# Performance work log

Measured on AMD Instinct MI355X. Metric: run time of the kernel, lower is better.

Reference implementation:

```python
import jax, jax.numpy as jnp
import numpy as np

N = 50000
E = 1600000
D_IN = 128
D_OUT = 128
K_EIG = 4
N_AGG = 3
N_SCALE = 3
AVG_D_LOG = float(np.log(33.0))  # avg_d['log'] for avg degree 32
BN_EPS = 1e-5


def setup_inputs() -> dict:
    key = jax.random.key(0)
    ks = jax.random.split(key, 8)
    h = jax.random.normal(ks[0], (N, D_IN), dtype=jnp.float32)
    eig = jax.random.normal(ks[1], (N, K_EIG), dtype=jnp.float32)
    snorm_n = jax.random.uniform(ks[2], (N, 1), dtype=jnp.float32)
    edge_src = jax.random.randint(ks[3], (E,), 0, N, dtype=jnp.int32)
    edge_dst = jax.random.randint(ks[4], (E,), 0, N, dtype=jnp.int32)
    d_cat = N_AGG * N_SCALE * D_IN  # 1152
    W = jax.random.normal(ks[5], (d_cat, D_OUT), dtype=jnp.float32) / np.sqrt(d_cat)
    b = jnp.zeros((D_OUT,), dtype=jnp.float32)
    bn_gamma = jnp.ones((D_OUT,), dtype=jnp.float32)
    bn_beta = jnp.zeros((D_OUT,), dtype=jnp.float32)
    bn_mean = jax.random.normal(ks[6], (D_OUT,), dtype=jnp.float32) * 0.1
    bn_var = jnp.ones((D_OUT,), dtype=jnp.float32)
    return {"h": h, "eig": eig, "snorm_n": snorm_n, "W": W, "b": b,
            "bn_gamma": bn_gamma, "bn_beta": bn_beta, "bn_mean": bn_mean,
            "bn_var": bn_var, "edge_src": edge_src, "edge_dst": edge_dst}


def reference(h, eig, snorm_n, W, b, bn_gamma, bn_beta, bn_mean, bn_var, edge_src, edge_dst):
    h_in = h
    # --- pretrans_edges: message e = src h; vector_field = eig_src - eig_dst ---
    h_e = h[edge_src]                      # [E, d] gathered edge messages
    vf = eig[edge_src] - eig[edge_dst]     # [E, k_eig]
    w = jnp.abs(vf[:, 0:1])                # dir1 weights [E, 1]

    # --- reduce: multi-aggregator segment reduce over destination nodes ---
    deg = jax.ops.segment_sum(jnp.ones((E,), h.dtype), edge_dst, num_segments=N)  # [N]
    deg_safe = jnp.maximum(deg, 1.0)
    sum_h = jax.ops.segment_sum(h_e, edge_dst, num_segments=N)
    mean_h = sum_h / deg_safe[:, None]
    max_h = jax.ops.segment_max(h_e, edge_dst, num_segments=N)
    max_h = jnp.where(deg[:, None] > 0, max_h, 0.0)  # empty mailbox -> 0
    dir_num = jax.ops.segment_sum(h_e * w, edge_dst, num_segments=N)
    dir_den = jax.ops.segment_sum(w, edge_dst, num_segments=N)  # [N, 1]
    dir_av = dir_num / (dir_den + 1e-30)
    agg = jnp.concatenate([mean_h, max_h, dir_av], axis=1)  # [N, 3d]

    # --- scalers: identity, amplification, attenuation ---
    logD = jnp.log(deg + 1.0)[:, None]
    amp = agg * (logD / AVG_D_LOG)
    att = agg * (AVG_D_LOG / jnp.maximum(logD, 1e-6))
    hcat = jnp.concatenate([agg, amp, att], axis=1)  # [N, 9d]

    # --- posttrans MLP (1 layer, no activation) ---
    out = hcat @ W + b
    # graph norm
    out = out * snorm_n
    # batch norm (eval mode, running stats)
    out = (out - bn_mean) * jax.lax.rsqrt(bn_var + BN_EPS) * bn_gamma + bn_beta
    out = jax.nn.relu(out)
    # residual (in_dim == out_dim)
    out = h_in + out
    # dropout p=0.0 / eval -> identity
    return out
```

## Files before the change

kernel.cpp:

```cpp
#include <hip/hip_runtime.h>
#include <hip/hip_bf16.h>

#define DIN 128
#define KEIG 4
#define BSH 7
#define BCAP 5120
#define ITEMS 16
#define AVG_D_LOG 3.4965075614664802f
#define BN_EPS 1e-5f

typedef __attribute__((ext_vector_type(8))) short bf16x8;
typedef __attribute__((ext_vector_type(4))) float f32x4;
typedef __attribute__((ext_vector_type(2))) float f32x2;

#define GLD16(SRC, DST) __builtin_amdgcn_global_load_lds(                     \
    (const __attribute__((address_space(1))) unsigned int*)(const void*)(SRC),\
    (__attribute__((address_space(3))) unsigned int*)(void*)(DST), 16, 0, 0)

static __device__ inline unsigned short f2bf(float f) {
    union { float f; unsigned u; } v; v.f = f;
    unsigned r = v.u + 0x7FFFu + ((v.u >> 16) & 1u);
    return (unsigned short)(r >> 16);
}
static __device__ inline unsigned pack2bf(float lo, float hi) {
    return (unsigned)f2bf(lo) | ((unsigned)f2bf(hi) << 16);
}
static __device__ inline f32x2 up2(unsigned u) {
    f32x2 r;
    r.x = __int_as_float(u << 16);
    r.y = __int_as_float(u & 0xffff0000u);
    return r;
}
static __device__ inline f32x2 pkmax(f32x2 a, f32x2 b) {
#if __has_builtin(__builtin_elementwise_max)
    return __builtin_elementwise_max(a, b);
#else
    a.x = fmaxf(a.x, b.x); a.y = fmaxf(a.y, b.y); return a;
#endif
}


__global__ void k_pb(const float* __restrict__ h, unsigned* __restrict__ hb,
                     const float* __restrict__ W, unsigned short* __restrict__ Wt,
                     const float* __restrict__ eig,
                     const int* __restrict__ src, const int* __restrict__ dst,
                     int* __restrict__ bcur, uint2* __restrict__ stag,
                     int nPairs, int wTotal, int E, int nbk, int gridB)
{
    __shared__ int lcnt[512];
    __shared__ int lbase[512];
    const int t = threadIdx.x;

    if ((int)blockIdx.x < gridB) {
        for (int b = t; b < nbk; b += 256) lcnt[b] = 0;
        __syncthreads();

        const int e0 = blockIdx.x * (256 * ITEMS);
        int   bky[ITEMS];
        int   rnk[ITEMS];
        uint2 rec[ITEMS];
#pragma unroll
        for (int k = 0; k < ITEMS; ++k) {
            const int e = e0 + t + k * 256;
            if (e < E) {
                const int s = src[e], d = dst[e];
                const float w = fabsf(eig[(size_t)s * KEIG] - eig[(size_t)d * KEIG]);
                rec[k] = make_uint2(((unsigned)f2bf(w) << 16) | (unsigned)s, (unsigned)d);
                bky[k] = d >> BSH;
                rnk[k] = atomicAdd(&lcnt[bky[k]], 1);
            } else bky[k] = -1;
        }
        __syncthreads();
        for (int b = t; b < nbk; b += 256) {
            const int c = lcnt[b];
            lbase[b] = c ? atomicAdd(&bcur[b], c) : 0;
        }
        __syncthreads();
#pragma unroll
        for (int k = 0; k < ITEMS; ++k) {
            if (bky[k] >= 0) {
                const int pos = lbase[bky[k]] + rnk[k];
                if (pos < BCAP) stag[(size_t)bky[k] * BCAP + pos] = rec[k];
            }
        }
    } else {
        const int i = ((int)blockIdx.x - gridB) * 256 + t;
        if (i < nPairs) {
            float2 v = reinterpret_cast<const float2*>(h)[i];
            hb[i] = pack2bf(v.x, v.y);
        }
        if (i < wTotal) {
            int k = i % 384;
            int rest = i / 384;
            int col = rest & 127;
            int s = rest >> 7;
            const int ks = k >> 5, kg = (k >> 3) & 3, ko = k & 7;
            const int c = s * 8 + kg * 2 + (col >> 6);
            const int lane = col & 63;
            const size_t idx = (size_t)ks * 12288 + c * 512 + lane * 8 + ko;
            Wt[idx] = f2bf(W[(s * 384 + k) * 128 + col]);
        }
    }
}


__global__ void k_group(const int* __restrict__ bcur, const uint2* __restrict__ stag,
                        unsigned* __restrict__ final_, int2* __restrict__ offcnt, int N)
{
    __shared__ uint2 sst[BCAP];
    __shared__ int hcnt[128];
    __shared__ int sbuf[2][128];
    const int b = blockIdx.x;
    const int t = threadIdx.x;
    const int cb = min(bcur[b], BCAP);

    for (int i = t; i < cb; i += 256) sst[i] = stag[(size_t)b * BCAP + i];
    if (t < 128) hcnt[t] = 0;
    __syncthreads();

    int dl[(BCAP + 255) / 256];
    int rk[(BCAP + 255) / 256];
    int nit = 0;
    for (int i = t; i < cb; i += 256) {
        const int d_loc = sst[i].y & 127;
        dl[nit] = d_loc;
        rk[nit] = atomicAdd(&hcnt[d_loc], 1);
        ++nit;
    }
    __syncthreads();

    int cur = 0;
    if (t < 128) sbuf[0][t] = hcnt[t];
    __syncthreads();
    for (int d = 1; d < 128; d <<= 1) {
        if (t < 128) {
            int x = sbuf[cur][t];
            if (t >= d) x += sbuf[cur][t - d];
            sbuf[cur ^ 1][t] = x;
        }
        cur ^= 1;
        __syncthreads();
    }
    const int exb = cur ^ 1;
    if (t < 128) sbuf[exb][t] = sbuf[cur][t] - hcnt[t];
    __syncthreads();

    if (t < 128) {
        const int dg = (b << BSH) + t;
        if (dg < N) offcnt[dg] = make_int2(b * BCAP + sbuf[exb][t], hcnt[t]);
    }
    nit = 0;
    for (int i = t; i < cb; i += 256) {
        final_[(size_t)b * BCAP + sbuf[exb][dl[nit]] + rk[nit]] = sst[i].x;
        ++nit;
    }
}


__global__ void k_prep(const float* __restrict__ h, unsigned* __restrict__ hb,
                       const float* __restrict__ W, unsigned short* __restrict__ Wt,
                       const float* __restrict__ eig, float* __restrict__ eig0,
                       int* __restrict__ cursor, int* __restrict__ bcur,
                       int nPairs, int wTotal, int N, int nbk)
{
    int i = blockIdx.x * 256 + threadIdx.x;
    if (i < nPairs) {
        float2 v = reinterpret_cast<const float2*>(h)[i];
        hb[i] = pack2bf(v.x, v.y);
    }
    if (i < wTotal) {
        int k = i % 384;
        int rest = i / 384;
        int col = rest & 127;
        int s = rest >> 7;
        const int ks = k >> 5, kg = (k >> 3) & 3, ko = k & 7;
        const int c = s * 8 + kg * 2 + (col >> 6);
        const int lane = col & 63;
        const size_t idx = (size_t)ks * 12288 + c * 512 + lane * 8 + ko;
        Wt[idx] = f2bf(W[(s * 384 + k) * 128 + col]);
    }
    if (i < N) {
        eig0[i] = eig[(size_t)i * KEIG];
        cursor[i] = 0;
    }
    if (i < nbk) bcur[i] = 0;
}

__global__ void k_hist(const int* __restrict__ dst, int* __restrict__ counts, int E) {
    int e = blockIdx.x * 256 + threadIdx.x;
    if (e < E) atomicAdd(&counts[dst[e]], 1);
}

__global__ void k_part(const int* __restrict__ counts, int* __restrict__ part, int N) {
    __shared__ int red[4];
    const int t = threadIdx.x;
    const int i = blockIdx.x * 256 + t;
    int v = (i < N) ? counts[i] : 0;
    for (int d = 32; d >= 1; d >>= 1) v += __shfl_down(v, d, 64);
    if ((t & 63) == 0) red[t >> 6] = v;
    __syncthreads();
    if (t == 0) part[blockIdx.x] = red[0] + red[1] + red[2] + red[3];
}

__global__ void k_scan1(const int* __restrict__ part, int* __restrict__ partoff,
                        int* __restrict__ total_out, int NB) {
    __shared__ int buf[2][256];
    const int t = threadIdx.x;
    int v = (t < NB) ? part[t] : 0;
    buf[0][t] = v;
    __syncthreads();
    int cur = 0;
    for (int d = 1; d < 256; d <<= 1) {
        int x = buf[cur][t];
        if (t >= d) x += buf[cur][t - d];
        buf[cur ^ 1][t] = x;
        cur ^= 1;
        __syncthreads();
    }
    if (t < NB) partoff[t] = buf[cur][t] - v;
    if (t == 255) *total_out = buf[cur][255];
}

__global__ void k_off(const int* __restrict__ counts, const int* __restrict__ partoff,
                      int* __restrict__ offsets, int* __restrict__ cursor, int N) {
    __shared__ int buf[2][256];
    const int t = threadIdx.x;
    const int i = blockIdx.x * 256 + t;
    int v = (i < N) ? counts[i] : 0;
    buf[0][t] = v;
    __syncthreads();
    int cur = 0;
    for (int d = 1; d < 256; d <<= 1) {
        int x = buf[cur][t];
        if (t >= d) x += buf[cur][t - d];
        buf[cur ^ 1][t] = x;
        cur ^= 1;
        __syncthreads();
    }
    if (i < N) {
        int excl = partoff[blockIdx.x] + buf[cur][t] - v;
        offsets[i] = excl;
        cursor[i]  = excl;
    }
}

__global__ void k_fill_csr(const int* __restrict__ src, const int* __restrict__ dst,
                           const float* __restrict__ eig0, int* __restrict__ cursor,
                           int2* __restrict__ sedge, int E)
{
    int e = blockIdx.x * 256 + threadIdx.x;
    if (e < E) {
        int s = src[e], d = dst[e];
        float w = fabsf(eig0[s] - eig0[d]);
        int pos = atomicAdd(&cursor[d], 1);
        sedge[pos] = make_int2(s, __float_as_int(w));
    }
}


template<bool PACKED>
__launch_bounds__(256, 4)
__global__ void k_agg(const unsigned* __restrict__ hb,
                      const int2* __restrict__ offcnt, const int* __restrict__ offsets,
                      const unsigned* __restrict__ upk, const int2* __restrict__ sedge,
                      unsigned short* __restrict__ agg, float2* __restrict__ scal, int N)
{
    const int tid = threadIdx.x;
    const int qid = tid >> 4;
    const int l16 = tid & 15;
    const int n = blockIdx.x * 16 + qid;
    if (n >= N) return;

    int e0, cnt;
    if (PACKED) { const int2 oc = offcnt[n]; e0 = oc.x; cnt = oc.y; }
    else        { e0 = offsets[n]; cnt = offsets[n + 1] - e0; }

    const uint4* __restrict__ hb4 = reinterpret_cast<const uint4*>(hb);

    f32x2 s2[4], m2[4], d2[4];
    float wsum = 0.f;
#pragma unroll
    for (int f = 0; f < 4; ++f) {
        s2[f] = (f32x2){0.f, 0.f};
        m2[f] = (f32x2){-INFINITY, -INFINITY};
        d2[f] = (f32x2){0.f, 0.f};
    }
    const int clampi = (cnt > 0) ? cnt - 1 : 0;

    uint4 bufA[8], bufB[8];
    float wvA[8], wvB[8];

#define STAGE(BUF, WV, BASE) do {                                        \
    _Pragma("unroll")                                                    \
    for (int j = 0; j < 8; ++j) {                                        \
        int ci = (BASE) + j; ci = ci < clampi ? ci : clampi;             \
        unsigned sidx;                                                   \
        if (PACKED) {                                                    \
            const unsigned u = upk[e0 + ci];                             \
            WV[j] = __int_as_float(u & 0xffff0000u);                     \
            sidx = (u & 0xffffu) << 4;                                   \
        } else {                                                         \
            const int2 v = sedge[e0 + ci];                               \
            WV[j] = __int_as_float(v.y);                                 \
            sidx = ((unsigned)v.x) << 4;                                 \
        }                                                                \
        BUF[j] = hb4[sidx | (unsigned)l16];                              \
    }                                                                    \
} while (0)

#define ACCUM(BUF, WV, BASE) do {                                        \
    _Pragma("unroll")                                                    \
    for (int j = 0; j < 8; ++j) {                                        \
        if ((BASE) + j < cnt) {                                          \
            const float wj = WV[j];                                      \
            const f32x2 wj2 = (f32x2){wj, wj};                           \
            const f32x2 p0 = up2(BUF[j].x), p1 = up2(BUF[j].y);          \
            const f32x2 p2 = up2(BUF[j].z), p3 = up2(BUF[j].w);          \
            s2[0] += p0; s2[1] += p1; s2[2] += p2; s2[3] += p3;          \
            m2[0] = pkmax(m2[0], p0); m2[1] = pkmax(m2[1], p1);          \
            m2[2] = pkmax(m2[2], p2); m2[3] = pkmax(m2[3], p3);          \
            d2[0] += p0 * wj2; d2[1] += p1 * wj2;                        \
            d2[2] += p2 * wj2; d2[3] += p3 * wj2;                        \
            wsum += wj;                                                  \
        }                                                                \
    }                                                                    \
} while (0)

    if (cnt > 0) {
        STAGE(bufA, wvA, 0);
        for (int base = 0; base < cnt; base += 16) {
            const bool haveB = (base + 8) < cnt;
            if (haveB) STAGE(bufB, wvB, base + 8);
            ACCUM(bufA, wvA, base);
            if (base + 16 < cnt) STAGE(bufA, wvA, base + 16);
            if (haveB) ACCUM(bufB, wvB, base + 8);
        }
    }
#undef STAGE
#undef ACCUM

    const float degf = (float)cnt;
    const float inv  = 1.0f / fmaxf(degf, 1.0f);
    const float dinv = 1.0f / (wsum + 1e-30f);
    const bool nz = (cnt > 0);
    uint4 pm, px, pd;
    pm.x = pack2bf(s2[0].x * inv, s2[0].y * inv);
    pm.y = pack2bf(s2[1].x * inv, s2[1].y * inv);
    pm.z = pack2bf(s2[2].x * inv, s2[2].y * inv);
    pm.w = pack2bf(s2[3].x * inv, s2[3].y * inv);
    px.x = pack2bf(nz ? m2[0].x : 0.f, nz ? m2[0].y : 0.f);
    px.y = pack2bf(nz ? m2[1].x : 0.f, nz ? m2[1].y : 0.f);
    px.z = pack2bf(nz ? m2[2].x : 0.f, nz ? m2[2].y : 0.f);
    px.w = pack2bf(nz ? m2[3].x : 0.f, nz ? m2[3].y : 0.f);
    pd.x = pack2bf(d2[0].x * dinv, d2[0].y * dinv);
    pd.y = pack2bf(d2[1].x * dinv, d2[1].y * dinv);
    pd.z = pack2bf(d2[2].x * dinv, d2[2].y * dinv);
    pd.w = pack2bf(d2[3].x * dinv, d2[3].y * dinv);

    uint4* aggv = reinterpret_cast<uint4*>(agg);
    const int mt = n >> 6, row = n & 63;
    const size_t b4 = (size_t)mt * 3072 + (size_t)(l16 & 3) * 64 + row;
    const int kshi = l16 >> 2;
    aggv[b4 + (size_t)(0 * 4 + kshi) * 256] = pm;
    aggv[b4 + (size_t)(1 * 4 + kshi) * 256] = px;
    aggv[b4 + (size_t)(2 * 4 + kshi) * 256] = pd;
    if (l16 == 0) {
        const float logD = logf(degf + 1.0f);
        scal[n] = make_float2(logD / AVG_D_LOG, AVG_D_LOG / fmaxf(logD, 1e-6f));
    }
}


__launch_bounds__(256, 2)
__global__ void k_mm(const unsigned short* __restrict__ agg, const float2* __restrict__ scal,
                     const float* __restrict__ h, const float* __restrict__ snorm,
                     const float* __restrict__ bvec, const float* __restrict__ gam,
                     const float* __restrict__ bet, const float* __restrict__ bmean,
                     const float* __restrict__ bvar, const unsigned short* __restrict__ Wt,
                     float* __restrict__ out, int N, int nT)
{
    __shared__ char smem[33792];
    unsigned short* As = (unsigned short*)smem;
    unsigned short* Bs = (unsigned short*)(smem + 8192);
    float* outS = (float*)smem;

    const int tid  = threadIdx.x;
    const int wave = tid >> 6;
    const int lane = tid & 63;
    const int r16  = lane & 15;
    const int kgrp = lane >> 4;
    const int cb = wave * 32;

    const int mt0 = blockIdx.x * 2;
    const int mt1 = (mt0 + 1 < nT) ? (mt0 + 1) : mt0;
    const char* aggb0 = (const char*)agg + (size_t)mt0 * 49152;
    const char* aggb1 = (const char*)agg + (size_t)mt1 * 49152;
    const char* wtbase = (const char*)Wt;

    auto stage = [&](int ks) {
        GLD16(aggb0 + (size_t)ks * 4096 + wave * 1024 + lane * 16,
              (char*)As + (size_t)wave * 1024);
        GLD16(aggb1 + (size_t)ks * 4096 + wave * 1024 + lane * 16,
              (char*)As + (size_t)(4 + wave) * 1024);
#pragma unroll
        for (int i = 0; i < 6; ++i) {
            const int c = wave * 6 + i;
            GLD16(wtbase + (size_t)ks * 24576 + (size_t)c * 1024 + lane * 16,
                  (char*)Bs + (size_t)c * 1024);
        }
    };

    f32x4 acc[2][4][2][3];
#pragma unroll
    for (int t = 0; t < 2; ++t)
#pragma unroll
        for (int m = 0; m < 4; ++m)
#pragma unroll
            for (int ct = 0; ct < 2; ++ct)
#pragma unroll
                for (int sv = 0; sv < 3; ++sv)
                    acc[t][m][ct][sv] = (f32x4){0.f, 0.f, 0.f, 0.f};

    for (int ks = 0; ks < 12; ++ks) {
        if (ks) __syncthreads();
        stage(ks);
        __syncthreads();

        bf16x8 a0[4], a1[4], b[6];
#pragma unroll
        for (int m = 0; m < 4; ++m) {
            a0[m] = *reinterpret_cast<const bf16x8*>(
                &As[((size_t)kgrp * 64 + m * 16 + r16) * 8]);
            a1[m] = *reinterpret_cast<const bf16x8*>(
                &As[((size_t)(4 + kgrp) * 64 + m * 16 + r16) * 8]);
        }
#pragma unroll
        for (int sv = 0; sv < 3; ++sv)
#pragma unroll
            for (int ct = 0; ct < 2; ++ct)
                b[sv * 2 + ct] = *reinterpret_cast<const bf16x8*>(
                    &Bs[(((size_t)sv * 4 + kgrp) * 128 + cb + ct * 16 + r16) * 8]);
#pragma unroll
        for (int sv = 0; sv < 3; ++sv)
#pragma unroll
            for (int ct = 0; ct < 2; ++ct)
#pragma unroll
                for (int m = 0; m < 4; ++m) {
                    acc[0][m][ct][sv] = __builtin_amdgcn_mfma_f32_16x16x32_bf16(
                        a0[m], b[sv * 2 + ct], acc[0][m][ct][sv], 0, 0, 0);
                    acc[1][m][ct][sv] = __builtin_amdgcn_mfma_f32_16x16x32_bf16(
                        a1[m], b[sv * 2 + ct], acc[1][m][ct][sv], 0, 0, 0);
                }
    }

    __syncthreads();
#pragma unroll
    for (int t = 0; t < 2; ++t) {
        if (t == 1 && mt1 == mt0) break;
        const int nb = (t ? mt1 : mt0) * 64;
#pragma unroll
        for (int ct = 0; ct < 2; ++ct) {
            const int col = cb + ct * 16 + r16;
            const float bc  = bvec[col];
            const float mc  = bmean[col];
            const float rs  = rsqrtf(bvar[col] + BN_EPS);
            const float gc  = gam[col];
            const float bec = bet[col];
#pragma unroll
            for (int m = 0; m < 4; ++m) {
#pragma unroll
                for (int r = 0; r < 4; ++r) {
                    const int row = m * 16 + kgrp * 4 + r;
                    const int n  = nb + row;
                    float sn = 0.f; float2 sc = make_float2(0.f, 0.f);
                    if (n < N) { sn = snorm[n]; sc = scal[n]; }
                    float v = acc[t][m][ct][0][r] + sc.x * acc[t][m][ct][1][r]
                                                  + sc.y * acc[t][m][ct][2][r];
                    float y = (v + bc) * sn;
                    y = (y - mc) * rs * gc + bec;
                    y = fmaxf(y, 0.f);
                    outS[row * 132 + col] = y;
                }
            }
        }
        __syncthreads();
        const int rows = (N - nb < 64) ? (N - nb) : 64;
#pragma unroll
        for (int it = 0; it < 8; ++it) {
            const int idx = it * 256 + tid;
            const int row = idx >> 5;
            const int c4  = idx & 31;
            if (row < rows) {
                const float4 hv = *reinterpret_cast<const float4*>(
                    &h[(size_t)(nb + row) * 128 + c4 * 4]);
                float4 yv = *reinterpret_cast<const float4*>(&outS[row * 132 + c4 * 4]);
                yv.x += hv.x; yv.y += hv.y; yv.z += hv.z; yv.w += hv.w;
                *reinterpret_cast<float4*>(&out[(size_t)(nb + row) * 128 + c4 * 4]) = yv;
            }
        }
        __syncthreads();
    }
}


extern "C" void kernel_launch(void* const* d_in, const int* in_sizes, int n_in,
                              void* d_out, int out_size, void* d_ws, size_t ws_size,
                              hipStream_t stream)
{
    const float* h     = (const float*)d_in[0];
    const float* eig   = (const float*)d_in[1];
    const float* snorm = (const float*)d_in[2];
    const float* W     = (const float*)d_in[3];
    const float* bvec  = (const float*)d_in[4];
    const float* gam   = (const float*)d_in[5];
    const float* bet   = (const float*)d_in[6];
    const float* bmean = (const float*)d_in[7];
    const float* bvar  = (const float*)d_in[8];
    const int*   esrc  = (const int*)d_in[9];
    const int*   edst  = (const int*)d_in[10];
    float* out = (float*)d_out;

    const int N = in_sizes[0] / DIN;
    const int E = in_sizes[9];
    const int NB = (N + 255) / 256;
    const int nPairs = N * DIN / 2;
    const int wTotal = 3 * 128 * 384;
    const int nbk = (N + 127) >> BSH;
    const int N64 = (N + 63) / 64;
    const int N128 = (N + 127) / 128;
    (void)ws_size; (void)n_in; (void)out_size;

    char* base = (char*)d_ws;
    size_t o = 0;
    auto take = [&](size_t bytes) {
        char* p = base + o;
        o = (o + bytes + 255) & ~(size_t)255;
        return p;
    };
    unsigned* hb       = (unsigned*)take((size_t)nPairs * 4);
    unsigned short* Wt = (unsigned short*)take((size_t)wTotal * 2);
    float* eig0        = (float*)take((size_t)N * 4);
    int* cursor        = (int*)take((size_t)(N + 1) * 4);
    float2* scal       = (float2*)take((size_t)N * 8);

    const size_t agg_bytes  = (size_t)N64 * 49152;
    const size_t stag_bytes = (size_t)nbk * BCAP * 8;
    const size_t shared_bytes = agg_bytes > stag_bytes ? agg_bytes : stag_bytes;

    const size_t bucket_bytes = (size_t)nbk * BCAP * 4
                              + (size_t)N * 8
                              + (size_t)nbk * 4
                              + shared_bytes + 8192;
    const bool bucketOK = (N <= 65536) && (nbk <= 512) && ((o + bucket_bytes) <= ws_size);

    const int gridPrep = (nPairs + 255) / 256;
    const int gridE    = (E + 255) / 256;
    const int gridB    = (E + 256 * ITEMS - 1) / (256 * ITEMS);
    const int gridN16  = (N + 15) / 16;

    if (bucketOK) {
        unsigned* fin   = (unsigned*)take((size_t)nbk * BCAP * 4);
        int2* offcnt    = (int2*)take((size_t)N * 8);
        int* bcur       = (int*)take((size_t)nbk * 4);
        char* shared    = take(shared_bytes);
        uint2* stag     = (uint2*)shared;
        unsigned short* agg = (unsigned short*)shared;

        hipMemsetAsync(bcur, 0, (size_t)nbk * 4, stream);
        k_pb<<<gridB + gridPrep, 256, 0, stream>>>(h, hb, W, Wt, eig, esrc, edst,
                                                   bcur, stag, nPairs, wTotal, E,
                                                   nbk, gridB);
        k_group<<<nbk, 256, 0, stream>>>(bcur, stag, fin, offcnt, N);
        k_agg<true><<<gridN16, 256, 0, stream>>>(hb, offcnt, nullptr, fin, nullptr,
                                                 agg, scal, N);
        k_mm<<<N128, 256, 0, stream>>>(agg, scal, h, snorm, bvec, gam, bet, bmean, bvar,
                                       Wt, out, N, N64);
    } else {
        int* counts  = (int*)take((size_t)(N + 1) * 4);
        int* offsets = (int*)take((size_t)(N + 1) * 4);
        int2* sedge  = (int2*)take((size_t)(E + 16) * 8);
        int* part    = (int*)take((size_t)NB * 4);
        int* partoff = (int*)take((size_t)NB * 4);
        int* bcur    = (int*)take(4096);
        unsigned short* agg = (unsigned short*)take(agg_bytes);

        k_prep<<<gridPrep, 256, 0, stream>>>(h, hb, W, Wt, eig, eig0, counts, bcur,
                                             nPairs, wTotal, N, 1);
        k_hist<<<gridE, 256, 0, stream>>>(edst, counts, E);
        k_part<<<NB, 256, 0, stream>>>(counts, part, N);
        k_scan1<<<1, 256, 0, stream>>>(part, partoff, &offsets[N], NB);
        k_off<<<NB, 256, 0, stream>>>(counts, partoff, offsets, cursor, N);
        k_fill_csr<<<gridE, 256, 0, stream>>>(esrc, edst, eig0, cursor, sedge, E);
        k_agg<false><<<gridN16, 256, 0, stream>>>(hb, nullptr, offsets, nullptr, sedge,
                                                  agg, scal, N);
        k_mm<<<N128, 256, 0, stream>>>(agg, scal, h, snorm, bvec, gam, bet, bmean, bvar,
                                       Wt, out, N, N64);
    }
}
```

Baseline: 151.8 us.

## Fuse bucket grouping with neighbor aggregation and shrink staging records

After: 167.3 us. 1.1x slower.

```diff
diff --git a/kernel.cpp b/kernel.cpp
--- a/kernel.cpp
+++ b/kernel.cpp
@@ -44,7 +44,8 @@
                      const float* __restrict__ W, unsigned short* __restrict__ Wt,
                      const float* __restrict__ eig,
                      const int* __restrict__ src, const int* __restrict__ dst,
-                     int* __restrict__ bcur, uint2* __restrict__ stag,
+                     int* __restrict__ bcur, unsigned* __restrict__ stagW,
+                     unsigned char* __restrict__ stagD,
                      int nPairs, int wTotal, int E, int nbk, int gridB)
 {
     __shared__ int lcnt[512];
@@ -56,16 +57,18 @@
         __syncthreads();
 
         const int e0 = blockIdx.x * (256 * ITEMS);
-        int   bky[ITEMS];
-        int   rnk[ITEMS];
-        uint2 rec[ITEMS];
+        int      bky[ITEMS];
+        int      rnk[ITEMS];
+        unsigned rw[ITEMS];
+        int      rd[ITEMS];
 #pragma unroll
         for (int k = 0; k < ITEMS; ++k) {
             const int e = e0 + t + k * 256;
             if (e < E) {
                 const int s = src[e], d = dst[e];
                 const float w = fabsf(eig[(size_t)s * KEIG] - eig[(size_t)d * KEIG]);
-                rec[k] = make_uint2(((unsigned)f2bf(w) << 16) | (unsigned)s, (unsigned)d);
+                rw[k] = ((unsigned)f2bf(w) << 16) | (unsigned)s;
+                rd[k] = d & ((1 << BSH) - 1);
                 bky[k] = d >> BSH;
                 rnk[k] = atomicAdd(&lcnt[bky[k]], 1);
             } else bky[k] = -1;
@@ -80,7 +83,10 @@
         for (int k = 0; k < ITEMS; ++k) {
             if (bky[k] >= 0) {
                 const int pos = lbase[bky[k]] + rnk[k];
-                if (pos < BCAP) stag[(size_t)bky[k] * BCAP + pos] = rec[k];
+                if (pos < BCAP) {
+                    stagW[(size_t)bky[k] * BCAP + pos] = rw[k];
+                    stagD[(size_t)bky[k] * BCAP + pos] = (unsigned char)rd[k];
+                }
             }
         }
     } else {
@@ -104,17 +110,26 @@
 }
 
 
-__global__ void k_group(const int* __restrict__ bcur, const uint2* __restrict__ stag,
-                        unsigned* __restrict__ final_, int2* __restrict__ offcnt, int N)
+__launch_bounds__(256)
+__global__ void k_ga(const unsigned* __restrict__ hb, const int* __restrict__ bcur,
+                     const unsigned* __restrict__ stagW,
+                     const unsigned char* __restrict__ stagD,
+                     unsigned short* __restrict__ agg, float2* __restrict__ scal, int N)
 {
-    __shared__ uint2 sst[BCAP];
+    __shared__ unsigned sW[BCAP];
+    __shared__ unsigned grpW[BCAP];
+    __shared__ unsigned char sD[BCAP];
     __shared__ int hcnt[128];
     __shared__ int sbuf[2][128];
+
     const int b = blockIdx.x;
     const int t = threadIdx.x;
     const int cb = min(bcur[b], BCAP);
 
-    for (int i = t; i < cb; i += 256) sst[i] = stag[(size_t)b * BCAP + i];
+    for (int i = t; i < cb; i += 256) {
+        sW[i] = stagW[(size_t)b * BCAP + i];
+        sD[i] = stagD[(size_t)b * BCAP + i];
+    }
     if (t < 128) hcnt[t] = 0;
     __syncthreads();
 
@@ -122,7 +137,7 @@
     int rk[(BCAP + 255) / 256];
     int nit = 0;
     for (int i = t; i < cb; i += 256) {
-        const int d_loc = sst[i].y & 127;
+        const int d_loc = sD[i];
         dl[nit] = d_loc;
         rk[nit] = atomicAdd(&hcnt[d_loc], 1);
         ++nit;
@@ -145,166 +160,45 @@
     if (t < 128) sbuf[exb][t] = sbuf[cur][t] - hcnt[t];
     __syncthreads();
 
-    if (t < 128) {
-        const int dg = (b << BSH) + t;
-        if (dg < N) offcnt[dg] = make_int2(b * BCAP + sbuf[exb][t], hcnt[t]);
-    }
     nit = 0;
     for (int i = t; i < cb; i += 256) {
-        final_[(size_t)b * BCAP + sbuf[exb][dl[nit]] + rk[nit]] = sst[i].x;
+        grpW[sbuf[exb][dl[nit]] + rk[nit]] = sW[i];
         ++nit;
     }
-}
-
-
-__global__ void k_prep(const float* __restrict__ h, unsigned* __restrict__ hb,
-                       const float* __restrict__ W, unsigned short* __restrict__ Wt,
-                       const float* __restrict__ eig, float* __restrict__ eig0,
-                       int* __restrict__ cursor, int* __restrict__ bcur,
-                       int nPairs, int wTotal, int N, int nbk)
-{
-    int i = blockIdx.x * 256 + threadIdx.x;
-    if (i < nPairs) {
-        float2 v = reinterpret_cast<const float2*>(h)[i];
-        hb[i] = pack2bf(v.x, v.y);
-    }
-    if (i < wTotal) {
-        int k = i % 384;
-        int rest = i / 384;
-        int col = rest & 127;
-        int s = rest >> 7;
-        const int ks = k >> 5, kg = (k >> 3) & 3, ko = k & 7;
-        const int c = s * 8 + kg * 2 + (col >> 6);
-        const int lane = col & 63;
-        const size_t idx = (size_t)ks * 12288 + c * 512 + lane * 8 + ko;
-        Wt[idx] = f2bf(W[(s * 384 + k) * 128 + col]);
-    }
-    if (i < N) {
-        eig0[i] = eig[(size_t)i * KEIG];
-        cursor[i] = 0;
-    }
-    if (i < nbk) bcur[i] = 0;
-}
-
-__global__ void k_hist(const int* __restrict__ dst, int* __restrict__ counts, int E) {
-    int e = blockIdx.x * 256 + threadIdx.x;
-    if (e < E) atomicAdd(&counts[dst[e]], 1);
-}
-
-__global__ void k_part(const int* __restrict__ counts, int* __restrict__ part, int N) {
-    __shared__ int red[4];
-    const int t = threadIdx.x;
-    const int i = blockIdx.x * 256 + t;
-    int v = (i < N) ? counts[i] : 0;
-    for (int d = 32; d >= 1; d >>= 1) v += __shfl_down(v, d, 64);
-    if ((t & 63) == 0) red[t >> 6] = v;
-    __syncthreads();
-    if (t == 0) part[blockIdx.x] = red[0] + red[1] + red[2] + red[3];
-}
-
-__global__ void k_scan1(const int* __restrict__ part, int* __restrict__ partoff,
-                        int* __restrict__ total_out, int NB) {
-    __shared__ int buf[2][256];
-    const int t = threadIdx.x;
-    int v = (t < NB) ? part[t] : 0;
-    buf[0][t] = v;
-    __syncthreads();
-    int cur = 0;
-    for (int d = 1; d < 256; d <<= 1) {
-        int x = buf[cur][t];
-        if (t >= d) x += buf[cur][t - d];
-        buf[cur ^ 1][t] = x;
-        cur ^= 1;
-        __syncthreads();
-    }
-    if (t < NB) partoff[t] = buf[cur][t] - v;
-    if (t == 255) *total_out = buf[cur][255];
-}
-
-__global__ void k_off(const int* __restrict__ counts, const int* __restrict__ partoff,
-                      int* __restrict__ offsets, int* __restrict__ cursor, int N) {
-    __shared__ int buf[2][256];
-    const int t = threadIdx.x;
-    const int i = blockIdx.x * 256 + t;
-    int v = (i < N) ? counts[i] : 0;
-    buf[0][t] = v;
-    __syncthreads();
-    int cur = 0;
-    for (int d = 1; d < 256; d <<= 1) {
-        int x = buf[cur][t];
-        if (t >= d) x += buf[cur][t - d];
-        buf[cur ^ 1][t] = x;
-        cur ^= 1;
-        __syncthreads();
-    }
-    if (i < N) {
-        int excl = partoff[blockIdx.x] + buf[cur][t] - v;
-        offsets[i] = excl;
-        cursor[i]  = excl;
-    }
-}
-
-__global__ void k_fill_csr(const int* __restrict__ src, const int* __restrict__ dst,
-                           const float* __restrict__ eig0, int* __restrict__ cursor,
-                           int2* __restrict__ sedge, int E)
-{
-    int e = blockIdx.x * 256 + threadIdx.x;
-    if (e < E) {
-        int s = src[e], d = dst[e];
-        float w = fabsf(eig0[s] - eig0[d]);
-        int pos = atomicAdd(&cursor[d], 1);
-        sedge[pos] = make_int2(s, __float_as_int(w));
-    }
-}
-
-
-template<bool PACKED>
-__launch_bounds__(256, 4)
-__global__ void k_agg(const unsigned* __restrict__ hb,
-                      const int2* __restrict__ offcnt, const int* __restrict__ offsets,
-                      const unsigned* __restrict__ upk, const int2* __restrict__ sedge,
-                      unsigned short* __restrict__ agg, float2* __restrict__ scal, int N)
-{
-    const int tid = threadIdx.x;
-    const int qid = tid >> 4;
-    const int l16 = tid & 15;
-    const int n = blockIdx.x * 16 + qid;
-    if (n >= N) return;
-
-    int e0, cnt;
-    if (PACKED) { const int2 oc = offcnt[n]; e0 = oc.x; cnt = oc.y; }
-    else        { e0 = offsets[n]; cnt = offsets[n + 1] - e0; }
-
+    __syncthreads();
+
+    const int qid = t >> 4;
+    const int l16 = t & 15;
     const uint4* __restrict__ hb4 = reinterpret_cast<const uint4*>(hb);
-
-    f32x2 s2[4], m2[4], d2[4];
-    float wsum = 0.f;
-#pragma unroll
-    for (int f = 0; f < 4; ++f) {
-        s2[f] = (f32x2){0.f, 0.f};
-        m2[f] = (f32x2){-INFINITY, -INFINITY};
-        d2[f] = (f32x2){0.f, 0.f};
-    }
-    const int clampi = (cnt > 0) ? cnt - 1 : 0;
-
-    uint4 bufA[8], bufB[8];
-    float wvA[8], wvB[8];
+    uint4* aggv = reinterpret_cast<uint4*>(agg);
+
+    for (int round = 0; round < 8; ++round) {
+        const int row = round * 16 + qid;
+        const int n = (b << BSH) + row;
+        if (n >= N) continue;
+        const int e0  = sbuf[exb][row];
+        const int cnt = hcnt[row];
+
+        f32x2 s2[4], m2[4], d2[4];
+        float wsum = 0.f;
+#pragma unroll
+        for (int f = 0; f < 4; ++f) {
+            s2[f] = (f32x2){0.f, 0.f};
+            m2[f] = (f32x2){-INFINITY, -INFINITY};
+            d2[f] = (f32x2){0.f, 0.f};
+        }
+        const int clampi = (cnt > 0) ? cnt - 1 : 0;
+
+        uint4 bufA[8], bufB[8];
+        float wvA[8], wvB[8];
 
 #define STAGE(BUF, WV, BASE) do {                                        \
     _Pragma("unroll")                                                    \
     for (int j = 0; j < 8; ++j) {                                        \
         int ci = (BASE) + j; ci = ci < clampi ? ci : clampi;             \
-        unsigned sidx;                                                   \
-        if (PACKED) {                                                    \
-            const unsigned u = upk[e0 + ci];                             \
-            WV[j] = __int_as_float(u & 0xffff0000u);                     \
-            sidx = (u & 0xffffu) << 4;                                   \
-        } else {                                                         \
-            const int2 v = sedge[e0 + ci];                               \
-            WV[j] = __int_as_float(v.y);                                 \
-            sidx = ((unsigned)v.x) << 4;                                 \
-        }                                                                \
-        BUF[j] = hb4[sidx | (unsigned)l16];                              \
+        const unsigned u = grpW[e0 + ci];                                \
+        WV[j] = __int_as_float(u & 0xffff0000u);                         \
+        BUF[j] = hb4[((u & 0xffffu) << 4) | (unsigned)l16];              \
     }                                                                    \
 } while (0)
 
@@ -326,6 +220,210 @@
     }                                                                    \
 } while (0)
 
+        if (cnt > 0) {
+            STAGE(bufA, wvA, 0);
+            for (int base = 0; base < cnt; base += 16) {
+                const bool haveB = (base + 8) < cnt;
+                if (haveB) STAGE(bufB, wvB, base + 8);
+                ACCUM(bufA, wvA, base);
+                if (base + 16 < cnt) STAGE(bufA, wvA, base + 16);
+                if (haveB) ACCUM(bufB, wvB, base + 8);
+            }
+        }
+#undef STAGE
+#undef ACCUM
+
+        const float degf = (float)cnt;
+        const float inv  = 1.0f / fmaxf(degf, 1.0f);
+        const float dinv = 1.0f / (wsum + 1e-30f);
+        const bool nz = (cnt > 0);
+        uint4 pm, px, pd;
+        pm.x = pack2bf(s2[0].x * inv, s2[0].y * inv);
+        pm.y = pack2bf(s2[1].x * inv, s2[1].y * inv);
+        pm.z = pack2bf(s2[2].x * inv, s2[2].y * inv);
+        pm.w = pack2bf(s2[3].x * inv, s2[3].y * inv);
+        px.x = pack2bf(nz ? m2[0].x : 0.f, nz ? m2[0].y : 0.f);
+        px.y = pack2bf(nz ? m2[1].x : 0.f, nz ? m2[1].y : 0.f);
+        px.z = pack2bf(nz ? m2[2].x : 0.f, nz ? m2[2].y : 0.f);
+        px.w = pack2bf(nz ? m2[3].x : 0.f, nz ? m2[3].y : 0.f);
+        pd.x = pack2bf(d2[0].x * dinv, d2[0].y * dinv);
+        pd.y = pack2bf(d2[1].x * dinv, d2[1].y * dinv);
+        pd.z = pack2bf(d2[2].x * dinv, d2[2].y * dinv);
+        pd.w = pack2bf(d2[3].x * dinv, d2[3].y * dinv);
+
+        const int mt = n >> 6, rowm = n & 63;
+        const size_t b4 = (size_t)mt * 3072 + (size_t)(l16 & 3) * 64 + rowm;
+        const int kshi = l16 >> 2;
+        aggv[b4 + (size_t)(0 * 4 + kshi) * 256] = pm;
+        aggv[b4 + (size_t)(1 * 4 + kshi) * 256] = px;
+        aggv[b4 + (size_t)(2 * 4 + kshi) * 256] = pd;
+        if (l16 == 0) {
+            const float logD = logf(degf + 1.0f);
+            scal[n] = make_float2(logD / AVG_D_LOG, AVG_D_LOG / fmaxf(logD, 1e-6f));
+        }
+    }
+}
+
+
+__global__ void k_prep(const float* __restrict__ h, unsigned* __restrict__ hb,
+                       const float* __restrict__ W, unsigned short* __restrict__ Wt,
+                       const float* __restrict__ eig, float* __restrict__ eig0,
+                       int* __restrict__ cursor, int* __restrict__ bcur,
+                       int nPairs, int wTotal, int N, int nbk)
+{
+    int i = blockIdx.x * 256 + threadIdx.x;
+    if (i < nPairs) {
+        float2 v = reinterpret_cast<const float2*>(h)[i];
+        hb[i] = pack2bf(v.x, v.y);
+    }
+    if (i < wTotal) {
+        int k = i % 384;
+        int rest = i / 384;
+        int col = rest & 127;
+        int s = rest >> 7;
+        const int ks = k >> 5, kg = (k >> 3) & 3, ko = k & 7;
+        const int c = s * 8 + kg * 2 + (col >> 6);
+        const int lane = col & 63;
+        const size_t idx = (size_t)ks * 12288 + c * 512 + lane * 8 + ko;
+        Wt[idx] = f2bf(W[(s * 384 + k) * 128 + col]);
+    }
+    if (i < N) {
+        eig0[i] = eig[(size_t)i * KEIG];
+        cursor[i] = 0;
+    }
+    if (i < nbk) bcur[i] = 0;
+}
+
+__global__ void k_hist(const int* __restrict__ dst, int* __restrict__ counts, int E) {
+    int e = blockIdx.x * 256 + threadIdx.x;
+    if (e < E) atomicAdd(&counts[dst[e]], 1);
+}
+
+__global__ void k_part(const int* __restrict__ counts, int* __restrict__ part, int N) {
+    __shared__ int red[4];
+    const int t = threadIdx.x;
+    const int i = blockIdx.x * 256 + t;
+    int v = (i < N) ? counts[i] : 0;
+    for (int d = 32; d >= 1; d >>= 1) v += __shfl_down(v, d, 64);
+    if ((t & 63) == 0) red[t >> 6] = v;
+    __syncthreads();
+    if (t == 0) part[blockIdx.x] = red[0] + red[1] + red[2] + red[3];
+}
+
+__global__ void k_scan1(const int* __restrict__ part, int* __restrict__ partoff,
+                        int* __restrict__ total_out, int NB) {
+    __shared__ int buf[2][256];
+    const int t = threadIdx.x;
+    int v = (t < NB) ? part[t] : 0;
+    buf[0][t] = v;
+    __syncthreads();
+    int cur = 0;
+    for (int d = 1; d < 256; d <<= 1) {
+        int x = buf[cur][t];
+        if (t >= d) x += buf[cur][t - d];
+        buf[cur ^ 1][t] = x;
+        cur ^= 1;
+        __syncthreads();
+    }
+    if (t < NB) partoff[t] = buf[cur][t] - v;
+    if (t == 255) *total_out = buf[cur][255];
+}
+
+__global__ void k_off(const int* __restrict__ counts, const int* __restrict__ partoff,
+                      int* __restrict__ offsets, int* __restrict__ cursor, int N) {
+    __shared__ int buf[2][256];
+    const int t = threadIdx.x;
+    const int i = blockIdx.x * 256 + t;
+    int v = (i < N) ? counts[i] : 0;
+    buf[0][t] = v;
+    __syncthreads();
+    int cur = 0;
+    for (int d = 1; d < 256; d <<= 1) {
+        int x = buf[cur][t];
+        if (t >= d) x += buf[cur][t - d];
+        buf[cur ^ 1][t] = x;
+        cur ^= 1;
+        __syncthreads();
+    }
+    if (i < N) {
+        int excl = partoff[blockIdx.x] + buf[cur][t] - v;
+        offsets[i] = excl;
+        cursor[i]  = excl;
+    }
+}
+
+__global__ void k_fill_csr(const int* __restrict__ src, const int* __restrict__ dst,
+                           const float* __restrict__ eig0, int* __restrict__ cursor,
+                           int2* __restrict__ sedge, int E)
+{
+    int e = blockIdx.x * 256 + threadIdx.x;
+    if (e < E) {
+        int s = src[e], d = dst[e];
+        float w = fabsf(eig0[s] - eig0[d]);
+        int pos = atomicAdd(&cursor[d], 1);
+        sedge[pos] = make_int2(s, __float_as_int(w));
+    }
+}
+
+__launch_bounds__(256, 4)
+__global__ void k_agg_csr(const unsigned* __restrict__ hb,
+                          const int* __restrict__ offsets, const int2* __restrict__ sedge,
+                          unsigned short* __restrict__ agg, float2* __restrict__ scal, int N)
+{
+    const int tid = threadIdx.x;
+    const int qid = tid >> 4;
+    const int l16 = tid & 15;
+    const int n = blockIdx.x * 16 + qid;
+    if (n >= N) return;
+
+    const int e0 = offsets[n];
+    const int cnt = offsets[n + 1] - e0;
+
+    const uint4* __restrict__ hb4 = reinterpret_cast<const uint4*>(hb);
+
+    f32x2 s2[4], m2[4], d2[4];
+    float wsum = 0.f;
+#pragma unroll
+    for (int f = 0; f < 4; ++f) {
+        s2[f] = (f32x2){0.f, 0.f};
+        m2[f] = (f32x2){-INFINITY, -INFINITY};
+        d2[f] = (f32x2){0.f, 0.f};
+    }
+    const int clampi = (cnt > 0) ? cnt - 1 : 0;
+    const int safe = (cnt > 0);
+
+    uint4 bufA[8], bufB[8];
+    float wvA[8], wvB[8];
+
+#define STAGE(BUF, WV, BASE) do {                                        \
+    _Pragma("unroll")                                                    \
+    for (int j = 0; j < 8; ++j) {                                        \
+        int ci = (BASE) + j; ci = ci < clampi ? ci : clampi;             \
+        const int2 v = sedge[e0 + ci];                                   \
+        WV[j] = __int_as_float(v.y);                                     \
+        const unsigned sidx = ((unsigned)(safe ? v.x : 0)) << 4;         \
+        BUF[j] = hb4[sidx | (unsigned)l16];                              \
+    }                                                                    \
+} while (0)
+
+#define ACCUM(BUF, WV, BASE) do {                                        \
+    _Pragma("unroll")                                                    \
+    for (int j = 0; j < 8; ++j) {                                        \
+        if ((BASE) + j < cnt) {                                          \
+            const float wj = WV[j];                                      \
+            const f32x2 wj2 = (f32x2){wj, wj};                           \
+            const f32x2 p0 = up2(BUF[j].x), p1 = up2(BUF[j].y);          \
+            const f32x2 p2 = up2(BUF[j].z), p3 = up2(BUF[j].w);          \
+            s2[0] += p0; s2[1] += p1; s2[2] += p2; s2[3] += p3;          \
+            m2[0] = pkmax(m2[0], p0); m2[1] = pkmax(m2[1], p1);          \
+            m2[2] = pkmax(m2[2], p2); m2[3] = pkmax(m2[3], p3);          \
+            d2[0] += p0 * wj2; d2[1] += p1 * wj2;                        \
+            d2[2] += p2 * wj2; d2[3] += p3 * wj2;                        \
+            wsum += wj;                                                  \
+        }                                                                \
+    }                                                                    \
+} while (0)
+
     if (cnt > 0) {
         STAGE(bufA, wvA, 0);
         for (int base = 0; base < cnt; base += 16) {
@@ -543,14 +641,12 @@
     int* cursor        = (int*)take((size_t)(N + 1) * 4);
     float2* scal       = (float2*)take((size_t)N * 8);
 
-    const size_t agg_bytes  = (size_t)N64 * 49152;
-    const size_t stag_bytes = (size_t)nbk * BCAP * 8;
-    const size_t shared_bytes = agg_bytes > stag_bytes ? agg_bytes : stag_bytes;
+    const size_t agg_bytes = (size_t)N64 * 49152;
 
     const size_t bucket_bytes = (size_t)nbk * BCAP * 4
-                              + (size_t)N * 8
+                              + (size_t)nbk * BCAP
                               + (size_t)nbk * 4
-                              + shared_bytes + 8192;
+                              + agg_bytes + 8192;
     const bool bucketOK = (N <= 65536) && (nbk <= 512) && ((o + bucket_bytes) <= ws_size);
 
     const int gridPrep = (nPairs + 255) / 256;
@@ -559,20 +655,16 @@
     const int gridN16  = (N + 15) / 16;
 
     if (bucketOK) {
-        unsigned* fin   = (unsigned*)take((size_t)nbk * BCAP * 4);
-        int2* offcnt    = (int2*)take((size_t)N * 8);
-        int* bcur       = (int*)take((size_t)nbk * 4);
-        char* shared    = take(shared_bytes);
-        uint2* stag     = (uint2*)shared;
-        unsigned short* agg = (unsigned short*)shared;
+        unsigned* stagW      = (unsigned*)take((size_t)nbk * BCAP * 4);
+        unsigned char* stagD = (unsigned char*)take((size_t)nbk * BCAP);
+        int* bcur            = (int*)take((size_t)nbk * 4);
+        unsigned short* agg  = (unsigned short*)take(agg_bytes);
 
         hipMemsetAsync(bcur, 0, (size_t)nbk * 4, stream);
         k_pb<<<gridB + gridPrep, 256, 0, stream>>>(h, hb, W, Wt, eig, esrc, edst,
-                                                   bcur, stag, nPairs, wTotal, E,
-                                                   nbk, gridB);
-        k_group<<<nbk, 256, 0, stream>>>(bcur, stag, fin, offcnt, N);
-        k_agg<true><<<gridN16, 256, 0, stream>>>(hb, offcnt, nullptr, fin, nullptr,
-                                                 agg, scal, N);
+                                                   bcur, stagW, stagD,
+                                                   nPairs, wTotal, E, nbk, gridB);
+        k_ga<<<nbk, 256, 0, stream>>>(hb, bcur, stagW, stagD, agg, scal, N);
         k_mm<<<N128, 256, 0, stream>>>(agg, scal, h, snorm, bvec, gam, bet, bmean, bvar,
                                        Wt, out, N, N64);
     } else {
@@ -591,8 +683,7 @@
         k_scan1<<<1, 256, 0, stream>>>(part, partoff, &offsets[N], NB);
         k_off<<<NB, 256, 0, stream>>>(counts, partoff, offsets, cursor, N);
         k_fill_csr<<<gridE, 256, 0, stream>>>(esrc, edst, eig0, cursor, sedge, E);
-        k_agg<false><<<gridN16, 256, 0, stream>>>(hb, nullptr, offsets, nullptr, sedge,
-                                                  agg, scal, N);
+        k_agg_csr<<<gridN16, 256, 0, stream>>>(hb, offsets, sedge, agg, scal, N);
         k_mm<<<N128, 256, 0, stream>>>(agg, scal, h, snorm, bvec, gam, bet, bmean, bvar,
                                        Wt, out, N, N64);
     }
```
